# Optimization experiments

Hardware: AMD Instinct MI355X
Metric: run time of the kernel (lower is better)

## Reference

```python
import jax, jax.numpy as jnp
import numpy as np

B, S, D, H = 2, 2048, 1024, 16
DH = D // H  # head_dim = 64


def setup_inputs() -> dict:
    key = jax.random.key(0)
    ks = jax.random.split(key, 10)
    inp = {
        "query": jax.random.normal(ks[0], (B, S, D), jnp.float32),
        "key": jax.random.normal(ks[1], (B, S, D), jnp.float32),
        "value": jax.random.normal(ks[2], (B, S, D), jnp.float32),
        "mask": jnp.ones((B, S), jnp.int32),
        # per-head q/k/v projections stacked over the head axis [H, D, DH]
        "Wq": jax.random.normal(ks[3], (H, D, DH), jnp.float32) * 0.02,
        "bq": jnp.zeros((H, DH), jnp.float32),
        "Wk": jax.random.normal(ks[4], (H, D, DH), jnp.float32) * 0.02,
        "bk": jnp.zeros((H, DH), jnp.float32),
        "Wv": jax.random.normal(ks[5], (H, D, DH), jnp.float32) * 0.02,
        "bv": jnp.zeros((H, DH), jnp.float32),
        # output projection fc: Linear(D, D)
        "Wo": jax.random.normal(ks[6], (D, D), jnp.float32) * 0.02,
        "bo": jnp.zeros((D,), jnp.float32),
    }
    return inp


def reference(query, key, value, mask, Wq, bq, Wk, bk, Wv, bv, Wo, bo):
    scale = 1.0 / jnp.sqrt(jnp.asarray(DH, query.dtype))
    # batched per-head projections: [B,S,D] x [H,D,DH] -> [B,H,S,DH]
    q = jnp.einsum('bsd,hde->bhse', query, Wq) + bq[None, :, None, :]
    k = jnp.einsum('bsd,hde->bhse', key, Wk) + bk[None, :, None, :]
    v = jnp.einsum('bsd,hde->bhse', value, Wv) + bv[None, :, None, :]
    # scaled dot-product attention scores [B,H,Sq,Sk]
    scores = jnp.einsum('bhqe,bhke->bhqk', q, k) * scale
    scores = jnp.where(mask[:, None, None, :] == 0, jnp.asarray(-1e9, scores.dtype), scores)
    attn = jax.nn.softmax(scores, axis=-1)
    ctx = jnp.einsum('bhqk,bhke->bhqe', attn, v)          # [B,H,S,DH]
    ctx = ctx.transpose(0, 2, 1, 3).reshape(query.shape[0], -1, H * DH)  # concat heads
    return ctx @ Wo + bo
```

## Files before the change

### kernel.cpp

```cpp
#include <hip/hip_runtime.h>
#include <stdint.h>
#include <math.h>


typedef __attribute__((ext_vector_type(8))) short short8;
typedef __attribute__((ext_vector_type(4))) float floatx4;

#define LOG2E 1.44269504088896340736f

__device__ __forceinline__ unsigned short f32_bf16(float f) {
  union { float f; unsigned u; } c; c.f = f;
  return (unsigned short)((c.u + 0x7FFFu + ((c.u >> 16) & 1u)) >> 16);
}
__device__ __forceinline__ float bf16_f32(unsigned short u) {
  union { unsigned u; float f; } c; c.u = ((unsigned)u) << 16;
  return c.f;
}
__device__ __forceinline__ void gld16(const void* g, void* l) {
  __builtin_amdgcn_global_load_lds((const __attribute__((address_space(1))) void*)g,
                                   (__attribute__((address_space(3))) void*)l, 16, 0, 0);
}


__global__ __launch_bounds__(256) void prep_kernel(
    const float* __restrict__ qf, const float* __restrict__ kf, const float* __restrict__ vf,
    const float* __restrict__ w0, const float* __restrict__ w1, const float* __restrict__ w2,
    const float* __restrict__ wo, const int* __restrict__ mask,
    unsigned short* __restrict__ oq, unsigned short* __restrict__ ok, unsigned short* __restrict__ ov,
    unsigned short* __restrict__ o0, unsigned short* __restrict__ o1, unsigned short* __restrict__ o2,
    unsigned short* __restrict__ oo, float* __restrict__ mb) {
  __shared__ float t[32][33];
  const int y = blockIdx.y, bx = blockIdx.x;
  if (y < 3) {
    if (y == 0 && bx < 16) {
      int j = bx * 256 + threadIdx.x;
      mb[j] = (mask[j] == 0) ? (-1.0e9f * LOG2E) : 0.0f;
    }
    const float* in = (y == 0) ? qf : (y == 1) ? kf : vf;
    unsigned short* out = (y == 0) ? oq : (y == 1) ? ok : ov;
    int i = bx * 256 + threadIdx.x;
    float4 v = reinterpret_cast<const float4*>(in)[i];
    ushort4 o;
    o.x = f32_bf16(v.x); o.y = f32_bf16(v.y); o.z = f32_bf16(v.z); o.w = f32_bf16(v.w);
    reinterpret_cast<ushort4*>(out)[i] = o;
    return;
  }
  const int tx = threadIdx.x & 31, ty = threadIdx.x >> 5;
  const float* in; unsigned short* out; int R, C, z, r0, c0;
  if (bx < 3072) {
    const int zb = bx >> 6, rem = bx & 63;
    const int sel = zb >> 4; z = zb & 15;
    in = (sel == 0) ? w0 : (sel == 1) ? w1 : w2;
    out = (sel == 0) ? o0 : (sel == 1) ? o1 : o2;
    R = 1024; C = 64; r0 = (rem >> 1) * 32; c0 = (rem & 1) * 32;
  } else {
    const int t2 = bx - 3072;
    in = wo; out = oo; R = 1024; C = 1024; z = 0;
    r0 = (t2 >> 5) * 32; c0 = (t2 & 31) * 32;
  }
  const float* inp = in + (size_t)z * R * C;
  #pragma unroll
  for (int j = 0; j < 4; ++j)
    t[ty + j * 8][tx] = inp[(size_t)(r0 + ty + j * 8) * C + c0 + tx];
  __syncthreads();
  #pragma unroll
  for (int j = 0; j < 4; ++j)
    out[((size_t)z * C + c0 + ty + j * 8) * R + r0 + tx] = f32_bf16(t[tx][ty + j * 8]);
}


__device__ __forceinline__ void gemm_core(
    const unsigned short* __restrict__ A, const unsigned short* __restrict__ Bt,
    int K, int blockM, int blockN,
    unsigned short* As, unsigned short* Bs, floatx4 acc[4][4]) {
  const int tid = threadIdx.x;
  const int w = tid >> 6;
  const int lane = tid & 63;
  const int quad = lane >> 4, l15 = lane & 15;
  const int wm = w & 1, wn = w >> 1;
  const int srow = lane >> 2;
  const int scol = (lane & 3) * 8;

  #pragma unroll
  for (int mi = 0; mi < 4; ++mi)
    #pragma unroll
    for (int ni = 0; ni < 4; ++ni)
      acc[mi][ni] = (floatx4){0.f, 0.f, 0.f, 0.f};

  const unsigned short* Arow = A + (size_t)blockM * K + (size_t)srow * K + scol;
  const unsigned short* Brow = Bt + (size_t)blockN * K + (size_t)srow * K + scol;

  auto stage = [&](int k0, int buf) {
    unsigned short* Asb = As + buf * (128 * 32);
    unsigned short* Bsb = Bs + buf * (128 * 32);
    #pragma unroll
    for (int i = 0; i < 2; ++i) {
      int row = w * 32 + i * 16;
      gld16(Arow + (size_t)row * K + k0, Asb + row * 32);
      gld16(Brow + (size_t)row * K + k0, Bsb + row * 32);
    }
  };

  const int iters = K >> 5;
  stage(0, 0);
  for (int it = 0; it < iters; ++it) {
    __syncthreads();
    if (it + 1 < iters) stage((it + 1) * 32, (it + 1) & 1);
    const unsigned short* Asb = As + (it & 1) * (128 * 32);
    const unsigned short* Bsb = Bs + (it & 1) * (128 * 32);
    short8 bf[4];
    #pragma unroll
    for (int ni = 0; ni < 4; ++ni)
      bf[ni] = *(const short8*)(Bsb + (wn * 64 + ni * 16 + l15) * 32 + quad * 8);
    #pragma unroll
    for (int mi = 0; mi < 4; ++mi) {
      short8 af = *(const short8*)(Asb + (wm * 64 + mi * 16 + l15) * 32 + quad * 8);
      #pragma unroll
      for (int ni = 0; ni < 4; ++ni)
        acc[mi][ni] = __builtin_amdgcn_mfma_f32_16x16x32_bf16(af, bf[ni], acc[mi][ni], 0, 0, 0);
    }
  }
}

__global__ __launch_bounds__(256) void gemm_proj_kernel(
    const unsigned short* __restrict__ qin, const unsigned short* __restrict__ kin,
    const unsigned short* __restrict__ vin,
    const unsigned short* __restrict__ WqT, const unsigned short* __restrict__ WkT,
    const unsigned short* __restrict__ WvT,
    const float* __restrict__ bq, const float* __restrict__ bk, const float* __restrict__ bv,
    unsigned short* __restrict__ Qp, unsigned short* __restrict__ Kp,
    unsigned short* __restrict__ Vt) {
  __shared__ unsigned short As[2][128 * 32];
  __shared__ unsigned short Bs[2][128 * 32];
  const int z = blockIdx.y, bx = blockIdx.x;
  const int r = bx & 7, j = bx >> 3;
  const unsigned short *A, *Bt;
  const float* bias;
  int blockM, blockN;
  if (z < 2) {
    blockM = (r * 4 + (j & 3)) * 128;
    blockN = (j >> 2) * 128;
    A = z ? kin : qin; Bt = z ? WkT : WqT; bias = z ? bk : bq;
  } else {
    blockN = (r * 4 + (j & 3)) * 128;
    blockM = (j >> 2) * 128;
    A = WvT; Bt = vin; bias = bv;
  }
  floatx4 acc[4][4];
  gemm_core(A, Bt, 1024, blockM, blockN, As[0], Bs[0], acc);

  const int tid = threadIdx.x, w = tid >> 6, lane = tid & 63;
  const int quad = lane >> 4, l15 = lane & 15;
  const int wm = w & 1, wn = w >> 1;

  if (z < 2) {
    unsigned short* outp = z ? Kp : Qp;
    #pragma unroll
    for (int mi = 0; mi < 4; ++mi)
      #pragma unroll
      for (int ni = 0; ni < 4; ++ni) {
        const int n = blockN + wn * 64 + ni * 16 + l15;
        const int h = n >> 6, e = n & 63;
        const float bvv = bias[n];
        #pragma unroll
        for (int rr = 0; rr < 4; ++rr) {
          const int m = blockM + wm * 64 + mi * 16 + quad * 4 + rr;
          const int b = m >> 11, s = m & 2047;
          outp[(((size_t)b * 16 + h) * 2048 + s) * 64 + e] = f32_bf16(acc[mi][ni][rr] + bvv);
        }
      }
  } else {
    #pragma unroll
    for (int mi = 0; mi < 4; ++mi) {
      float br[4];
      #pragma unroll
      for (int rr = 0; rr < 4; ++rr)
        br[rr] = bias[blockM + wm * 64 + mi * 16 + quad * 4 + rr];
      #pragma unroll
      for (int ni = 0; ni < 4; ++ni) {
        const int n = blockN + wn * 64 + ni * 16 + l15;
        const int b = n >> 11, s = n & 2047;
        #pragma unroll
        for (int rr = 0; rr < 4; ++rr) {
          const int m = blockM + wm * 64 + mi * 16 + quad * 4 + rr;
          const int h = m >> 6, e = m & 63;
          Vt[(((size_t)b * 16 + h) * 64 + e) * 2048 + s] = f32_bf16(acc[mi][ni][rr] + br[rr]);
        }
      }
    }
  }
}

__global__ __launch_bounds__(256) void gemm_out_kernel(
    const unsigned short* __restrict__ A, const unsigned short* __restrict__ Bt,
    const float* __restrict__ bias, float* __restrict__ out, int K, int N) {
  __shared__ unsigned short As[2][128 * 32];
  __shared__ unsigned short Bs[2][64 * 32];
  const int tid = threadIdx.x;
  const int w = tid >> 6, lane = tid & 63;
  const int quad = lane >> 4, l15 = lane & 15;
  const int wm = w & 1, wn = w >> 1;
  const int srow = lane >> 2;
  const int scol = (lane & 3) * 8;
  const int l = blockIdx.x, r = l & 7, j = l >> 3;
  const int blockM = (r * 4 + (j & 3)) * 128;
  const int blockN = (j >> 2) * 64;

  floatx4 acc[4][2];
  #pragma unroll
  for (int mi = 0; mi < 4; ++mi)
    #pragma unroll
    for (int ni = 0; ni < 2; ++ni)
      acc[mi][ni] = (floatx4){0.f, 0.f, 0.f, 0.f};

  const unsigned short* Arow = A + (size_t)blockM * K + (size_t)srow * K + scol;
  const unsigned short* Brow = Bt + (size_t)blockN * K + (size_t)srow * K + scol;

  auto stage = [&](int k0, int buf) {
    #pragma unroll
    for (int i = 0; i < 2; ++i) {
      int row = w * 32 + i * 16;
      gld16(Arow + (size_t)row * K + k0, As[buf] + row * 32);
    }
    gld16(Brow + (size_t)(w * 16) * K + k0, Bs[buf] + (w * 16) * 32);
  };

  const int iters = K >> 5;
  stage(0, 0);
  for (int it = 0; it < iters; ++it) {
    __syncthreads();
    if (it + 1 < iters) stage((it + 1) * 32, (it + 1) & 1);
    const unsigned short* Asb = As[it & 1];
    const unsigned short* Bsb = Bs[it & 1];
    short8 bf[2];
    #pragma unroll
    for (int ni = 0; ni < 2; ++ni)
      bf[ni] = *(const short8*)(Bsb + (wn * 32 + ni * 16 + l15) * 32 + quad * 8);
    #pragma unroll
    for (int mi = 0; mi < 4; ++mi) {
      short8 af = *(const short8*)(Asb + (wm * 64 + mi * 16 + l15) * 32 + quad * 8);
      #pragma unroll
      for (int ni = 0; ni < 2; ++ni)
        acc[mi][ni] = __builtin_amdgcn_mfma_f32_16x16x32_bf16(af, bf[ni], acc[mi][ni], 0, 0, 0);
    }
  }

  #pragma unroll
  for (int mi = 0; mi < 4; ++mi)
    #pragma unroll
    for (int ni = 0; ni < 2; ++ni) {
      const int n = blockN + wn * 32 + ni * 16 + l15;
      const float bv = bias[n];
      #pragma unroll
      for (int rr = 0; rr < 4; ++rr) {
        const int m = blockM + wm * 64 + mi * 16 + quad * 4 + rr;
        out[(size_t)m * N + n] = acc[mi][ni][rr] + bv;
      }
    }
}


__global__ __launch_bounds__(256) void attn_kernel(
    const unsigned short* __restrict__ Q, const unsigned short* __restrict__ Kg,
    const unsigned short* __restrict__ Vt, const float* __restrict__ maskAdd,
    unsigned short* __restrict__ ctx) {
  const int S = 2048;
  const int tid = threadIdx.x;
  const int w = tid >> 6, lane = tid & 63, quad = lane >> 4, l15 = lane & 15;
  const int l = blockIdx.x, r8 = l & 7, j8 = l >> 3;
  const int bh = r8 * 4 + (j8 & 3);
  const int qb = j8 >> 2;
  const int b = bh >> 4, h = bh & 15;
  const int q0 = qb * 128;

  __shared__ unsigned short Ks[2][128 * 64];
  __shared__ unsigned short Vs[2][64 * 128];
  __shared__ unsigned short Ps[4][32 * 64];
  unsigned short* Pw = Ps[w];

  const unsigned short* Qb = Q + (size_t)bh * S * 64;
  const unsigned short* Kb = Kg + (size_t)bh * S * 64;
  const unsigned short* Vb = Vt + (size_t)bh * 64 * S;
  const float* mb = maskAdd + (size_t)b * S;

  const float qs = 0.125f * LOG2E;
  short8 qf[2][2];
  #pragma unroll
  for (int mi = 0; mi < 2; ++mi)
    #pragma unroll
    for (int kq = 0; kq < 2; ++kq) {
      short8 v = *(const short8*)(Qb + (size_t)(q0 + w * 32 + mi * 16 + l15) * 64 + kq * 32 + quad * 8);
      #pragma unroll
      for (int jj = 0; jj < 8; ++jj)
        v[jj] = (short)f32_bf16(bf16_f32((unsigned short)v[jj]) * qs);
      qf[mi][kq] = v;
    }

  short8 onesf;
  #pragma unroll
  for (int jj = 0; jj < 8; ++jj) onesf[jj] = (short)0x3F80;

  floatx4 O[2][4], ls[2];
  #pragma unroll
  for (int mi = 0; mi < 2; ++mi) {
    #pragma unroll
    for (int ne = 0; ne < 4; ++ne) O[mi][ne] = (floatx4){0.f, 0.f, 0.f, 0.f};
    ls[mi] = (floatx4){0.f, 0.f, 0.f, 0.f};
  }

  auto stage_kv = [&](int t, int buf) {
    const int kv0 = t * 128;
    #pragma unroll
    for (int i = 0; i < 4; ++i) {
      int r0 = w * 32 + i * 8;
      int row = r0 + (lane >> 3);
      int cg = (lane & 7) ^ (row & 7);
      gld16(Kb + (size_t)(kv0 + row) * 64 + cg * 8, Ks[buf] + r0 * 64);
    }
    #pragma unroll
    for (int i = 0; i < 4; ++i) {
      int r0 = w * 16 + i * 4;
      int row = r0 + (lane >> 4);
      int p = lane & 15;
      int cg = (p & 8) | ((p & 7) ^ (row & 7));
      gld16(Vb + (size_t)row * S + kv0 + cg * 8, Vs[buf] + r0 * 128);
    }
  };

  stage_kv(0, 0);
  for (int t = 0; t < 16; ++t) {
    const int kv0 = t * 128;
    __syncthreads();
    float ma[8];
    #pragma unroll
    for (int ni = 0; ni < 8; ++ni) ma[ni] = mb[kv0 + ni * 16 + l15];
    if (t + 1 < 16) stage_kv(t + 1, (t + 1) & 1);
    const unsigned short* Ksb = Ks[t & 1];
    const unsigned short* Vsb = Vs[t & 1];

    #pragma unroll
    for (int ph = 0; ph < 2; ++ph) {
      floatx4 sc[2][4];
      #pragma unroll
      for (int ni = 0; ni < 4; ++ni) {
        const int key = (ph * 4 + ni) * 16 + l15;
        short8 kf0 = *(const short8*)(Ksb + key * 64 + ((quad) ^ (l15 & 7)) * 8);
        short8 kf1 = *(const short8*)(Ksb + key * 64 + ((4 + quad) ^ (l15 & 7)) * 8);
        #pragma unroll
        for (int mi = 0; mi < 2; ++mi) {
          floatx4 s = (floatx4){0.f, 0.f, 0.f, 0.f};
          s = __builtin_amdgcn_mfma_f32_16x16x32_bf16(qf[mi][0], kf0, s, 0, 0, 0);
          s = __builtin_amdgcn_mfma_f32_16x16x32_bf16(qf[mi][1], kf1, s, 0, 0, 0);
          sc[mi][ni] = s;
        }
      }
      #pragma unroll
      for (int mi = 0; mi < 2; ++mi)
        #pragma unroll
        for (int rr = 0; rr < 4; ++rr) {
          const int row = mi * 16 + quad * 4 + rr;
          const int g = (row + (row >> 3)) & 7;
          #pragma unroll
          for (int ni = 0; ni < 4; ++ni) {
            float p = __builtin_amdgcn_exp2f(sc[mi][ni][rr] + ma[ph * 4 + ni]);
            union { float f; unsigned u; } c; c.f = p;
            const int ch = (ni * 2 + (l15 >> 3)) ^ g;
            Pw[row * 64 + (ch & 7) * 8 + (l15 & 7)] = (unsigned short)(c.u >> 16);
          }
        }
      #pragma unroll
      for (int kkl = 0; kkl < 2; ++kkl) {
        const int kk = ph * 2 + kkl;
        short8 pfr[2], vfr[4];
        #pragma unroll
        for (int mi = 0; mi < 2; ++mi) {
          const int gp = (2 * mi + l15 + (l15 >> 3)) & 7;
          pfr[mi] = *(const short8*)(Pw + (mi * 16 + l15) * 64 + ((kkl * 4 + quad) ^ gp) * 8);
        }
        #pragma unroll
        for (int ne = 0; ne < 4; ++ne) {
          const int c = kk * 4 + quad;
          vfr[ne] = *(const short8*)(Vsb + (ne * 16 + l15) * 128 + ((c & 8) | ((c & 7) ^ (l15 & 7))) * 8);
        }
        #pragma unroll
        for (int mi = 0; mi < 2; ++mi) {
          #pragma unroll
          for (int ne = 0; ne < 4; ++ne)
            O[mi][ne] = __builtin_amdgcn_mfma_f32_16x16x32_bf16(pfr[mi], vfr[ne], O[mi][ne], 0, 0, 0);
          ls[mi] = __builtin_amdgcn_mfma_f32_16x16x32_bf16(pfr[mi], onesf, ls[mi], 0, 0, 0);
        }
      }
    }
  }

  #pragma unroll
  for (int mi = 0; mi < 2; ++mi)
    #pragma unroll
    for (int rr = 0; rr < 4; ++rr) {
      const float inv = __builtin_amdgcn_rcpf(ls[mi][rr]);
      const int s = q0 + w * 32 + mi * 16 + quad * 4 + rr;
      #pragma unroll
      for (int ne = 0; ne < 4; ++ne)
        ctx[((size_t)b * S + s) * 1024 + h * 64 + ne * 16 + l15] = f32_bf16(O[mi][ne][rr] * inv);
    }
}


extern "C" void kernel_launch(void* const* d_in, const int* in_sizes, int n_in,
                              void* d_out, int out_size, void* d_ws, size_t ws_size,
                              hipStream_t stream) {
  const float* query = (const float*)d_in[0];
  const float* key   = (const float*)d_in[1];
  const float* value = (const float*)d_in[2];
  const int*   mask  = (const int*)d_in[3];
  const float* Wq = (const float*)d_in[4];
  const float* bq = (const float*)d_in[5];
  const float* Wk = (const float*)d_in[6];
  const float* bk = (const float*)d_in[7];
  const float* Wv = (const float*)d_in[8];
  const float* bv = (const float*)d_in[9];
  const float* Wo = (const float*)d_in[10];
  const float* bo = (const float*)d_in[11];
  float* out = (float*)d_out;

  char* ws = (char*)d_ws;
  const size_t MB = 1024 * 1024;
  unsigned short* qin  = (unsigned short*)(ws + 0);
  unsigned short* kin  = (unsigned short*)(ws + 8 * MB);
  unsigned short* vin  = (unsigned short*)(ws + 16 * MB);
  unsigned short* WqT  = (unsigned short*)(ws + 24 * MB);
  unsigned short* WkT  = (unsigned short*)(ws + 26 * MB);
  unsigned short* WvT  = (unsigned short*)(ws + 28 * MB);
  unsigned short* WoT  = (unsigned short*)(ws + 30 * MB);
  unsigned short* Qp   = (unsigned short*)(ws + 32 * MB);
  unsigned short* Kp   = (unsigned short*)(ws + 40 * MB);
  unsigned short* Vt   = (unsigned short*)(ws + 48 * MB);
  float* maskAdd       = (float*)(ws + 56 * MB);
  unsigned short* ctxb = qin;

  prep_kernel<<<dim3(4096, 4), 256, 0, stream>>>(query, key, value, Wq, Wk, Wv, Wo, mask,
                                                 qin, kin, vin, WqT, WkT, WvT, WoT, maskAdd);
  gemm_proj_kernel<<<dim3(256, 3), 256, 0, stream>>>(qin, kin, vin, WqT, WkT, WvT,
                                                     bq, bk, bv, Qp, Kp, Vt);
  attn_kernel<<<dim3(512), 256, 0, stream>>>(Qp, Kp, Vt, maskAdd, ctxb);
  gemm_out_kernel<<<dim3(512), 256, 0, stream>>>(ctxb, WoT, bo, out, 1024, 1024);
}
```

Measured before the change: 241.3 us.

## Rewrite projection GEMM with 256x256 tiles, swizzled LDS, and staged epilogue

The QKV projection GEMM now runs as 192 blocks of 512 threads, each computing a 256x256 tile with a K-step of 64 instead of 768 blocks computing 128x128 tiles with a K-step of 32. LDS rows use an XOR swizzle to avoid bank conflicts, and the MFMA work is split into phases separated by barriers with raised wave priority so LDS reads interleave with matrix math. The epilogue writes results into swizzled LDS first and then does coalesced 16-byte stores, replacing scattered 2-byte global stores, which matters most for the transposed V output. The cost is 128KB of shared memory per block and fewer blocks, 192 on a GPU with about 256 CUs, which leaves some CUs idle.

```diff
diff --git a/kernel.cpp b/kernel.cpp
--- a/kernel.cpp
+++ b/kernel.cpp
@@ -69,60 +69,7 @@
 }
 
 
-__device__ __forceinline__ void gemm_core(
-    const unsigned short* __restrict__ A, const unsigned short* __restrict__ Bt,
-    int K, int blockM, int blockN,
-    unsigned short* As, unsigned short* Bs, floatx4 acc[4][4]) {
-  const int tid = threadIdx.x;
-  const int w = tid >> 6;
-  const int lane = tid & 63;
-  const int quad = lane >> 4, l15 = lane & 15;
-  const int wm = w & 1, wn = w >> 1;
-  const int srow = lane >> 2;
-  const int scol = (lane & 3) * 8;
-
-  #pragma unroll
-  for (int mi = 0; mi < 4; ++mi)
-    #pragma unroll
-    for (int ni = 0; ni < 4; ++ni)
-      acc[mi][ni] = (floatx4){0.f, 0.f, 0.f, 0.f};
-
-  const unsigned short* Arow = A + (size_t)blockM * K + (size_t)srow * K + scol;
-  const unsigned short* Brow = Bt + (size_t)blockN * K + (size_t)srow * K + scol;
-
-  auto stage = [&](int k0, int buf) {
-    unsigned short* Asb = As + buf * (128 * 32);
-    unsigned short* Bsb = Bs + buf * (128 * 32);
-    #pragma unroll
-    for (int i = 0; i < 2; ++i) {
-      int row = w * 32 + i * 16;
-      gld16(Arow + (size_t)row * K + k0, Asb + row * 32);
-      gld16(Brow + (size_t)row * K + k0, Bsb + row * 32);
-    }
-  };
-
-  const int iters = K >> 5;
-  stage(0, 0);
-  for (int it = 0; it < iters; ++it) {
-    __syncthreads();
-    if (it + 1 < iters) stage((it + 1) * 32, (it + 1) & 1);
-    const unsigned short* Asb = As + (it & 1) * (128 * 32);
-    const unsigned short* Bsb = Bs + (it & 1) * (128 * 32);
-    short8 bf[4];
-    #pragma unroll
-    for (int ni = 0; ni < 4; ++ni)
-      bf[ni] = *(const short8*)(Bsb + (wn * 64 + ni * 16 + l15) * 32 + quad * 8);
-    #pragma unroll
-    for (int mi = 0; mi < 4; ++mi) {
-      short8 af = *(const short8*)(Asb + (wm * 64 + mi * 16 + l15) * 32 + quad * 8);
-      #pragma unroll
-      for (int ni = 0; ni < 4; ++ni)
-        acc[mi][ni] = __builtin_amdgcn_mfma_f32_16x16x32_bf16(af, bf[ni], acc[mi][ni], 0, 0, 0);
-    }
-  }
-}
-
-__global__ __launch_bounds__(256) void gemm_proj_kernel(
+__global__ __launch_bounds__(512, 2) void gemm_proj_kernel(
     const unsigned short* __restrict__ qin, const unsigned short* __restrict__ kin,
     const unsigned short* __restrict__ vin,
     const unsigned short* __restrict__ WqT, const unsigned short* __restrict__ WkT,
@@ -130,63 +77,199 @@
     const float* __restrict__ bq, const float* __restrict__ bk, const float* __restrict__ bv,
     unsigned short* __restrict__ Qp, unsigned short* __restrict__ Kp,
     unsigned short* __restrict__ Vt) {
-  __shared__ unsigned short As[2][128 * 32];
-  __shared__ unsigned short Bs[2][128 * 32];
-  const int z = blockIdx.y, bx = blockIdx.x;
-  const int r = bx & 7, j = bx >> 3;
-  const unsigned short *A, *Bt;
-  const float* bias;
-  int blockM, blockN;
-  if (z < 2) {
-    blockM = (r * 4 + (j & 3)) * 128;
-    blockN = (j >> 2) * 128;
-    A = z ? kin : qin; Bt = z ? WkT : WqT; bias = z ? bk : bq;
-  } else {
-    blockN = (r * 4 + (j & 3)) * 128;
-    blockM = (j >> 2) * 128;
-    A = WvT; Bt = vin; bias = bv;
-  }
-  floatx4 acc[4][4];
-  gemm_core(A, Bt, 1024, blockM, blockN, As[0], Bs[0], acc);
-
-  const int tid = threadIdx.x, w = tid >> 6, lane = tid & 63;
+  __shared__ unsigned short As[2][2][128 * 64];
+  __shared__ unsigned short Bs[2][2][128 * 64];
+
+  const int z = blockIdx.y;
+  const int x = blockIdx.x;
+  const int r = x & 7, q = x >> 3;
+  int mt, nt;
+  if (z < 2) { mt = r * 2 + (q >> 2); nt = q & 3; }
+  else       { nt = r * 2 + (q >> 2); mt = q & 3; }
+  const int blockM = mt * 256, blockN = nt * 256;
+
+  const unsigned short* A  = (z == 0) ? qin : (z == 1) ? kin : WvT;
+  const unsigned short* Bt = (z == 0) ? WqT : (z == 1) ? WkT : vin;
+  const float* bias = (z == 0) ? bq : (z == 1) ? bk : bv;
+
+  const int tid = threadIdx.x;
+  const int w = tid >> 6, lane = tid & 63;
   const int quad = lane >> 4, l15 = lane & 15;
   const int wm = w & 1, wn = w >> 1;
 
+  const int lr8 = lane >> 3;
+  const int lc8 = lane & 7;
+  const int gcs = lc8 ^ lr8;
+
+  auto stage = [&](int k0, int buf) {
+    #pragma unroll
+    for (int h = 0; h < 2; ++h)
+      #pragma unroll
+      for (int s2 = 0; s2 < 2; ++s2) {
+        const int rl = s2 * 64 + w * 8;
+        gld16(A + (size_t)(blockM + h * 128 + rl + lr8) * 1024 + k0 + gcs * 8,
+              &As[buf][h][rl * 64]);
+      }
+    #pragma unroll
+    for (int h = 0; h < 2; ++h)
+      #pragma unroll
+      for (int s2 = 0; s2 < 2; ++s2) {
+        const int rl = s2 * 64 + w * 8;
+        gld16(Bt + (size_t)(blockN + h * 128 + rl + lr8) * 1024 + k0 + gcs * 8,
+              &Bs[buf][h][rl * 64]);
+      }
+  };
+
+  floatx4 acc[8][4];
+  #pragma unroll
+  for (int mi = 0; mi < 8; ++mi)
+    #pragma unroll
+    for (int ni = 0; ni < 4; ++ni)
+      acc[mi][ni] = (floatx4){0.f, 0.f, 0.f, 0.f};
+
+  stage(0, 0);
+  __syncthreads();
+
+  const int brb = (wn & 1) * 64;
+
+  for (int st = 0; st < 16; ++st) {
+    const int buf = st & 1;
+    const unsigned short* Ah = &As[buf][wm][0];
+    const unsigned short* Bh = &Bs[buf][wn >> 1][0];
+    short8 af[4][2], b0[2][2], b1[2][2];
+
+    if (st + 1 < 16) stage((st + 1) * 64, buf ^ 1);
+    #pragma unroll
+    for (int mi = 0; mi < 4; ++mi) {
+      const int row = mi * 16 + l15;
+      #pragma unroll
+      for (int kk = 0; kk < 2; ++kk)
+        af[mi][kk] = *(const short8*)(Ah + row * 64 + (((kk * 4 + quad) ^ (row & 7)) << 3));
+    }
+    #pragma unroll
+    for (int ni = 0; ni < 2; ++ni) {
+      const int row = brb + ni * 16 + l15;
+      #pragma unroll
+      for (int kk = 0; kk < 2; ++kk)
+        b0[ni][kk] = *(const short8*)(Bh + row * 64 + (((kk * 4 + quad) ^ (row & 7)) << 3));
+    }
+    __builtin_amdgcn_s_barrier();
+    __builtin_amdgcn_s_setprio(1);
+    #pragma unroll
+    for (int mi = 0; mi < 4; ++mi)
+      #pragma unroll
+      for (int ni = 0; ni < 2; ++ni)
+        #pragma unroll
+        for (int kk = 0; kk < 2; ++kk)
+          acc[mi][ni] = __builtin_amdgcn_mfma_f32_16x16x32_bf16(af[mi][kk], b0[ni][kk], acc[mi][ni], 0, 0, 0);
+    __builtin_amdgcn_s_setprio(0);
+    __builtin_amdgcn_s_barrier();
+
+    #pragma unroll
+    for (int ni = 0; ni < 2; ++ni) {
+      const int row = brb + (ni + 2) * 16 + l15;
+      #pragma unroll
+      for (int kk = 0; kk < 2; ++kk)
+        b1[ni][kk] = *(const short8*)(Bh + row * 64 + (((kk * 4 + quad) ^ (row & 7)) << 3));
+    }
+    __builtin_amdgcn_s_barrier();
+    __builtin_amdgcn_s_setprio(1);
+    #pragma unroll
+    for (int mi = 0; mi < 4; ++mi)
+      #pragma unroll
+      for (int ni = 0; ni < 2; ++ni)
+        #pragma unroll
+        for (int kk = 0; kk < 2; ++kk)
+          acc[mi][ni + 2] = __builtin_amdgcn_mfma_f32_16x16x32_bf16(af[mi][kk], b1[ni][kk], acc[mi][ni + 2], 0, 0, 0);
+    __builtin_amdgcn_s_setprio(0);
+    __builtin_amdgcn_s_barrier();
+
+    #pragma unroll
+    for (int mi = 0; mi < 4; ++mi) {
+      const int row = (mi + 4) * 16 + l15;
+      #pragma unroll
+      for (int kk = 0; kk < 2; ++kk)
+        af[mi][kk] = *(const short8*)(Ah + row * 64 + (((kk * 4 + quad) ^ (row & 7)) << 3));
+    }
+    __builtin_amdgcn_s_barrier();
+    __builtin_amdgcn_s_setprio(1);
+    #pragma unroll
+    for (int mi = 0; mi < 4; ++mi)
+      #pragma unroll
+      for (int ni = 0; ni < 2; ++ni)
+        #pragma unroll
+        for (int kk = 0; kk < 2; ++kk)
+          acc[mi + 4][ni + 2] = __builtin_amdgcn_mfma_f32_16x16x32_bf16(af[mi][kk], b1[ni][kk], acc[mi + 4][ni + 2], 0, 0, 0);
+    __builtin_amdgcn_s_setprio(0);
+    __builtin_amdgcn_s_barrier();
+
+    __builtin_amdgcn_s_setprio(1);
+    #pragma unroll
+    for (int mi = 0; mi < 4; ++mi)
+      #pragma unroll
+      for (int ni = 0; ni < 2; ++ni)
+        #pragma unroll
+        for (int kk = 0; kk < 2; ++kk)
+          acc[mi + 4][ni] = __builtin_amdgcn_mfma_f32_16x16x32_bf16(af[mi][kk], b0[ni][kk], acc[mi + 4][ni], 0, 0, 0);
+    __builtin_amdgcn_s_setprio(0);
+    __syncthreads();
+  }
+
+  unsigned short* Cw = (w < 4) ? ((unsigned short*)As + w * 8192)
+                               : ((unsigned short*)Bs + (w - 4) * 8192);
+  const int pc = lc8 ^ lr8;
+
   if (z < 2) {
     unsigned short* outp = z ? Kp : Qp;
-    #pragma unroll
-    for (int mi = 0; mi < 4; ++mi)
-      #pragma unroll
-      for (int ni = 0; ni < 4; ++ni) {
-        const int n = blockN + wn * 64 + ni * 16 + l15;
-        const int h = n >> 6, e = n & 63;
-        const float bvv = bias[n];
+    const int n0 = blockN + wn * 64;
+    const int m0 = blockM + wm * 128;
+    float bn[4];
+    #pragma unroll
+    for (int ni = 0; ni < 4; ++ni) bn[ni] = bias[n0 + ni * 16 + l15];
+    #pragma unroll
+    for (int mi = 0; mi < 8; ++mi)
+      #pragma unroll
+      for (int ni = 0; ni < 4; ++ni)
         #pragma unroll
         for (int rr = 0; rr < 4; ++rr) {
-          const int m = blockM + wm * 64 + mi * 16 + quad * 4 + rr;
-          const int b = m >> 11, s = m & 2047;
-          outp[(((size_t)b * 16 + h) * 2048 + s) * 64 + e] = f32_bf16(acc[mi][ni][rr] + bvv);
-        }
-      }
+          const int row = mi * 16 + quad * 4 + rr;
+          const int col = ni * 16 + l15;
+          Cw[row * 64 + (((col >> 3) ^ (row & 7)) << 3) + (col & 7)] =
+              f32_bf16(acc[mi][ni][rr] + bn[ni]);
+        }
+    const size_t bb = (size_t)(m0 >> 11);
+    const int h = n0 >> 6, s0 = m0 & 2047;
+    unsigned short* dst = outp + ((bb * 16 + h) * 2048 + s0) * 64;
+    #pragma unroll
+    for (int ps = 0; ps < 16; ++ps) {
+      const int lr = ps * 8 + lr8;
+      *(short8*)(dst + lr * 64 + lc8 * 8) = *(const short8*)(Cw + lr * 64 + pc * 8);
+    }
   } else {
-    #pragma unroll
-    for (int mi = 0; mi < 4; ++mi) {
-      float br[4];
-      #pragma unroll
-      for (int rr = 0; rr < 4; ++rr)
-        br[rr] = bias[blockM + wm * 64 + mi * 16 + quad * 4 + rr];
-      #pragma unroll
-      for (int ni = 0; ni < 4; ++ni) {
-        const int n = blockN + wn * 64 + ni * 16 + l15;
-        const int b = n >> 11, s = n & 2047;
+    const int m0 = blockM + wm * 128;
+    const int n0 = blockN + wn * 64;
+    #pragma unroll
+    for (int mi = 0; mi < 8; ++mi) {
+      float bm[4];
+      #pragma unroll
+      for (int rr = 0; rr < 4; ++rr) bm[rr] = bias[m0 + mi * 16 + quad * 4 + rr];
+      #pragma unroll
+      for (int ni = 0; ni < 4; ++ni)
         #pragma unroll
         for (int rr = 0; rr < 4; ++rr) {
-          const int m = blockM + wm * 64 + mi * 16 + quad * 4 + rr;
-          const int h = m >> 6, e = m & 63;
-          Vt[(((size_t)b * 16 + h) * 64 + e) * 2048 + s] = f32_bf16(acc[mi][ni][rr] + br[rr]);
-        }
-      }
+          const int row = mi * 16 + quad * 4 + rr;
+          const int col = ni * 16 + l15;
+          Cw[row * 64 + (((col >> 3) ^ (row & 7)) << 3) + (col & 7)] =
+              f32_bf16(acc[mi][ni][rr] + bm[rr]);
+        }
+    }
+    const size_t bb = (size_t)(n0 >> 11);
+    const int s0 = n0 & 2047;
+    unsigned short* dst = Vt + (bb * 1024 + m0) * 2048 + s0;
+    #pragma unroll
+    for (int ps = 0; ps < 16; ++ps) {
+      const int lr = ps * 8 + lr8;
+      *(short8*)(dst + (size_t)lr * 2048 + lc8 * 8) = *(const short8*)(Cw + lr * 64 + pc * 8);
     }
   }
 }
@@ -440,8 +523,8 @@
 
   prep_kernel<<<dim3(4096, 4), 256, 0, stream>>>(query, key, value, Wq, Wk, Wv, Wo, mask,
                                                  qin, kin, vin, WqT, WkT, WvT, WoT, maskAdd);
-  gemm_proj_kernel<<<dim3(256, 3), 256, 0, stream>>>(qin, kin, vin, WqT, WkT, WvT,
-                                                     bq, bk, bv, Qp, Kp, Vt);
+  gemm_proj_kernel<<<dim3(64, 3), 512, 0, stream>>>(qin, kin, vin, WqT, WkT, WvT,
+                                                    bq, bk, bv, Qp, Kp, Vt);
   attn_kernel<<<dim3(512), 256, 0, stream>>>(Qp, Kp, Vt, maskAdd, ctxb);
   gemm_out_kernel<<<dim3(512), 256, 0, stream>>>(ctxb, WoT, bo, out, 1024, 1024);
 }
```

After: 231.0 us. 4.3% less time.
